# Kernel tuning notes

Measured on AMD Instinct MI355X. Metric: run time of the kernel, lower is better.

The kernel has to match this reference:

```python
import jax, jax.numpy as jnp
import numpy as np

N, E, H, L, G = 50000, 800000, 128, 4, 64

def setup_inputs() -> dict:
    key = jax.random.key(0)
    ks = jax.random.split(key, 16)
    s = 0.05
    x = jax.random.normal(ks[0], (N, H), jnp.float32)
    edge_index = jax.random.randint(ks[1], (2, E), 0, N)
    edge_attr = jax.random.normal(ks[2], (E, 1), jnp.float32)
    # sorted graph assignment covering all G graphs (batch[-1]+1 == G)
    batch = (jnp.arange(N) * G) // N
    conv_W1 = jax.random.normal(ks[3], (L, H, H), jnp.float32) * s
    conv_b1 = jnp.zeros((L, H), jnp.float32)
    conv_W2 = jax.random.normal(ks[4], (L, H, H), jnp.float32) * s
    conv_b2 = jnp.zeros((L, H), jnp.float32)
    conv_eps = jnp.zeros((L,), jnp.float32)  # torch init: eps = 0
    edge_W = jax.random.normal(ks[5], (L, 1, H), jnp.float32) * s
    edge_b = jnp.zeros((L, H), jnp.float32)
    vn_W1 = jax.random.normal(ks[6], (L - 1, H, H), jnp.float32) * s
    vn_b1 = jnp.zeros((L - 1, H), jnp.float32)
    vn_W2 = jax.random.normal(ks[7], (L - 1, H, H), jnp.float32) * s
    vn_b2 = jnp.zeros((L - 1, H), jnp.float32)
    vn_emb = jnp.zeros((H,), jnp.float32)  # torch init: constant 0
    return dict(x=x, edge_attr=edge_attr, conv_W1=conv_W1, conv_b1=conv_b1,
                conv_W2=conv_W2, conv_b2=conv_b2, conv_eps=conv_eps,
                edge_W=edge_W, edge_b=edge_b, vn_W1=vn_W1, vn_b1=vn_b1,
                vn_W2=vn_W2, vn_b2=vn_b2, vn_emb=vn_emb,
                edge_index=edge_index, batch=batch)


def reference(x, edge_attr, conv_W1, conv_b1, conv_W2, conv_b2, conv_eps,
              edge_W, edge_b, vn_W1, vn_b1, vn_W2, vn_b2, vn_emb,
              edge_index, batch):
    src, tgt = edge_index[0], edge_index[1]
    # PyG mean aggregation: divide scatter-sum by in-degree (clamped to 1)
    deg = jnp.maximum(
        jax.ops.segment_sum(jnp.ones((E,), x.dtype), tgt, num_segments=N), 1.0)[:, None]
    vn = jnp.broadcast_to(vn_emb[None, :], (G, H))  # virtual node per graph
    h = x
    hs = []
    for i in range(L):
        h = h + vn[batch]
        edge_emb = edge_attr @ edge_W[i] + edge_b[i]          # [E,H]
        msg = jax.nn.relu(h[src] + edge_emb)                   # gather + relu
        agg = jax.ops.segment_sum(msg, tgt, num_segments=N) / deg  # mean scatter
        z = (1.0 + conv_eps[i]) * h + agg
        h = jax.nn.relu(z @ conv_W1[i] + conv_b1[i]) @ conv_W2[i] + conv_b2[i]
        hs.append(h)
        if i < L - 1:
            vt = jax.ops.segment_sum(hs[i], batch, num_segments=G) + vn
            vn = jax.nn.relu(
                jax.nn.relu(vt @ vn_W1[i] + vn_b1[i]) @ vn_W2[i] + vn_b2[i])
            # eval mode: dropout is identity
    return jnp.concatenate(hs, axis=1)  # [N, L*H] jumping-knowledge concat
```

## Files before the change

### kernel.cpp

```cpp
#include <hip/hip_runtime.h>

#define NN 50000
#define EE 800000
#define HH 128
#define LL 4
#define GG 64
#define NR 50048

typedef short bf16x8 __attribute__((ext_vector_type(8)));
typedef float f32x4 __attribute__((ext_vector_type(4)));

__device__ __forceinline__ unsigned bf_round(float f) {
  unsigned u = __float_as_uint(f);
  return (u + 0x7fffu + ((u >> 16) & 1u)) >> 16;
}
__device__ __forceinline__ unsigned bf_pack2(float lo, float hi) {
  return bf_round(lo) | (bf_round(hi) << 16);
}

__global__ __launch_bounds__(256) void count_kernel(const int* __restrict__ tgt,
                                                    int* __restrict__ cnt, int E) {
  int e = blockIdx.x * 256 + threadIdx.x;
  if (e < E) atomicAdd(&cnt[tgt[e]], 1);
}

__global__ __launch_bounds__(256) void blocksum_kernel(const int* __restrict__ cnt,
                                                       int* __restrict__ bs, int N) {
  int i = blockIdx.x * 256 + threadIdx.x;
  int v = (i < N) ? cnt[i] : 0;
  __shared__ int sm[256];
  sm[threadIdx.x] = v;
  __syncthreads();
  for (int s = 128; s >= 1; s >>= 1) {
    if (threadIdx.x < s) sm[threadIdx.x] += sm[threadIdx.x + s];
    __syncthreads();
  }
  if (threadIdx.x == 0) bs[blockIdx.x] = sm[0];
}

__global__ __launch_bounds__(256) void bs_scan_kernel(int* __restrict__ bs, int nb) {
  __shared__ int sm[256];
  int t = threadIdx.x;
  int v = (t < nb) ? bs[t] : 0;
  sm[t] = v;
  __syncthreads();
  for (int off = 1; off < 256; off <<= 1) {
    int u = (t >= off) ? sm[t - off] : 0;
    __syncthreads();
    sm[t] += u;
    __syncthreads();
  }
  if (t < nb) bs[t] = sm[t] - v;
  if (t == 255) bs[nb] = sm[255];
}

__global__ __launch_bounds__(256) void blockscan_kernel(const int* __restrict__ cnt,
                                                        const int* __restrict__ bs,
                                                        int* __restrict__ rp, int N, int nb) {
  int b = blockIdx.x, t = threadIdx.x;
  int i = b * 256 + t;
  int v = (i < N) ? cnt[i] : 0;
  __shared__ int sm[256];
  sm[t] = v;
  __syncthreads();
  for (int off = 1; off < 256; off <<= 1) {
    int u = (t >= off) ? sm[t - off] : 0;
    __syncthreads();
    sm[t] += u;
    __syncthreads();
  }
  if (i < N) rp[i] = sm[t] - v + bs[b];
  if (b == 0 && t == 0) rp[N] = bs[nb];
}

__global__ __launch_bounds__(256) void scatter_kernel(const int* __restrict__ src,
                                                      const int* __restrict__ tgt,
                                                      const float* __restrict__ attr,
                                                      const int* __restrict__ rp,
                                                      int* __restrict__ cur,
                                                      int2* __restrict__ es, int E) {
  int e = blockIdx.x * 256 + threadIdx.x;
  if (e < E) {
    int t = tgt[e];
    int p = rp[t] + atomicAdd(&cur[t], 1);
    int2 rec;
    rec.x = src[e];
    rec.y = __float_as_int(attr[e]);
    es[p] = rec;
  }
}

__global__ __launch_bounds__(256) void vn_init_kernel(const float* __restrict__ emb,
                                                      float* __restrict__ vn, int total) {
  int i = blockIdx.x * 256 + threadIdx.x;
  if (i < total) vn[i] = emb[i & (HH - 1)];
}

__global__ __launch_bounds__(256) void wtconv_kernel(const float* __restrict__ W1,
                                                     const float* __restrict__ W2,
                                                     short* __restrict__ wt1,
                                                     short* __restrict__ wt2) {
  int idx = blockIdx.x * 256 + threadIdx.x;
  int m = idx >> 14;
  int r = idx & 16383;
  int n = r >> 7, k = r & 127;
  const float* W = (m < LL) ? (W1 + (size_t)m * 16384) : (W2 + (size_t)(m - LL) * 16384);
  short* D = (m < LL) ? (wt1 + (size_t)m * 16384) : (wt2 + (size_t)(m - LL) * 16384);
  D[n * 128 + k] = (short)bf_round(W[k * 128 + n]);
}

__global__ __launch_bounds__(256) void pack_kernel(const float4* __restrict__ hp, int pitch4,
                                                   const float4* __restrict__ vn,
                                                   const int* __restrict__ batch,
                                                   uint2* __restrict__ hbf, int N) {
  int idx = blockIdx.x * 256 + threadIdx.x;
  if (idx >= N * (HH / 4)) return;
  int n = idx >> 5;
  int c4 = idx & 31;
  int g = batch[n];
  float4 a = hp[(size_t)n * pitch4 + c4];
  float4 b = vn[g * 32 + c4];
  uint2 o;
  o.x = bf_pack2(a.x + b.x, a.y + b.y);
  o.y = bf_pack2(a.z + b.z, a.w + b.w);
  hbf[idx] = o;
}

__global__ __launch_bounds__(128) void agg_kernel(const unsigned* __restrict__ hbf,
                                                  const float2* __restrict__ hp2, int pitch2,
                                                  const float2* __restrict__ vn2,
                                                  const int* __restrict__ batch,
                                                  const int2* __restrict__ es,
                                                  const int* __restrict__ rp,
                                                  const float2* __restrict__ eW2,
                                                  const float2* __restrict__ eb2,
                                                  const float* __restrict__ epsp,
                                                  unsigned* __restrict__ zb, int N) {
  int wave = threadIdx.x >> 6;
  int lane = threadIdx.x & 63;
  int n = blockIdx.x * 2 + wave;
  if (n >= N) return;
  float2 ew = eW2[lane];
  float2 eb = eb2[lane];
  int rs = rp[n], re = rp[n + 1];
  float acc0 = 0.f, acc1 = 0.f;
  int k = rs;
  for (; k + 8 <= re; k += 8) {
    int2 e[8];
    unsigned p[8];
#pragma unroll
    for (int u = 0; u < 8; ++u) e[u] = es[k + u];
#pragma unroll
    for (int u = 0; u < 8; ++u) p[u] = hbf[((unsigned)e[u].x << 6) + lane];
#pragma unroll
    for (int u = 0; u < 8; ++u) {
      float a = __int_as_float(e[u].y);
      acc0 += fmaxf(__uint_as_float(p[u] << 16) + fmaf(a, ew.x, eb.x), 0.f);
      acc1 += fmaxf(__uint_as_float(p[u] & 0xffff0000u) + fmaf(a, ew.y, eb.y), 0.f);
    }
  }
  for (; k + 4 <= re; k += 4) {
    int2 e[4];
    unsigned p[4];
#pragma unroll
    for (int u = 0; u < 4; ++u) e[u] = es[k + u];
#pragma unroll
    for (int u = 0; u < 4; ++u) p[u] = hbf[((unsigned)e[u].x << 6) + lane];
#pragma unroll
    for (int u = 0; u < 4; ++u) {
      float a = __int_as_float(e[u].y);
      acc0 += fmaxf(__uint_as_float(p[u] << 16) + fmaf(a, ew.x, eb.x), 0.f);
      acc1 += fmaxf(__uint_as_float(p[u] & 0xffff0000u) + fmaf(a, ew.y, eb.y), 0.f);
    }
  }
  for (; k < re; ++k) {
    int2 e = es[k];
    unsigned p = hbf[((unsigned)e.x << 6) + lane];
    float a = __int_as_float(e.y);
    acc0 += fmaxf(__uint_as_float(p << 16) + fmaf(a, ew.x, eb.x), 0.f);
    acc1 += fmaxf(__uint_as_float(p & 0xffff0000u) + fmaf(a, ew.y, eb.y), 0.f);
  }
  int g = batch[n];
  float2 h = hp2[(size_t)n * pitch2 + lane];
  float2 v = vn2[(size_t)g * 64 + lane];
  float hs0 = h.x + v.x;
  float hs1 = h.y + v.y;
  float inv = 1.f / fmaxf((float)(re - rs), 1.f);
  float onep = 1.f + epsp[0];
  float o0 = fmaf(onep, hs0, acc0 * inv);
  float o1 = fmaf(onep, hs1, acc1 * inv);
  zb[(size_t)n * 64 + lane] = bf_pack2(o0, o1);
}

__global__ __launch_bounds__(256) void mlp_kernel(const unsigned* __restrict__ zb,
                                                  const short* __restrict__ wt1,
                                                  const float* __restrict__ b1,
                                                  const short* __restrict__ wt2,
                                                  const float* __restrict__ b2,
                                                  float* __restrict__ out, int layer, int N) {
  __shared__ char smem[64 * 272];
  int tid = threadIdx.x;
  int w = tid >> 6, lane = tid & 63;
  int l15 = lane & 15, q = lane >> 4;
  int row0 = blockIdx.x * 64;
  int wrow = w * 16;

  const uint4* z4 = (const uint4*)zb;
#pragma unroll
  for (int it = 0; it < 4; ++it) {
    int f = lane + it * 64;
    int r = f >> 4, c16 = f & 15;
    uint4 v = z4[(size_t)(row0 + wrow + r) * 16 + c16];
    *(uint4*)(&smem[(wrow + r) * 272 + c16 * 16]) = v;
  }

  f32x4 zero = {0.f, 0.f, 0.f, 0.f};
  f32x4 acc[8];
#pragma unroll
  for (int j = 0; j < 8; ++j) acc[j] = zero;

#pragma unroll
  for (int s = 0; s < 4; ++s) {
    bf16x8 af = *(const bf16x8*)(&smem[(wrow + l15) * 272 + (s * 32 + q * 8) * 2]);
#pragma unroll
    for (int j = 0; j < 8; ++j) {
      bf16x8 bf = *(const bf16x8*)(wt1 + (size_t)(j * 16 + l15) * 128 + s * 32 + q * 8);
      acc[j] = __builtin_amdgcn_mfma_f32_16x16x32_bf16(af, bf, acc[j], 0, 0, 0);
    }
  }
#pragma unroll
  for (int j = 0; j < 8; ++j) {
    float bv = b1[j * 16 + l15];
#pragma unroll
    for (int r = 0; r < 4; ++r) {
      float v = fmaxf(acc[j][r] + bv, 0.f);
      *(short*)(&smem[(wrow + q * 4 + r) * 272 + (j * 16 + l15) * 2]) = (short)bf_round(v);
    }
    acc[j] = zero;
  }
#pragma unroll
  for (int s = 0; s < 4; ++s) {
    bf16x8 af = *(const bf16x8*)(&smem[(wrow + l15) * 272 + (s * 32 + q * 8) * 2]);
#pragma unroll
    for (int j = 0; j < 8; ++j) {
      bf16x8 bf = *(const bf16x8*)(wt2 + (size_t)(j * 16 + l15) * 128 + s * 32 + q * 8);
      acc[j] = __builtin_amdgcn_mfma_f32_16x16x32_bf16(af, bf, acc[j], 0, 0, 0);
    }
  }
#pragma unroll
  for (int j = 0; j < 8; ++j) {
    float bv = b2[j * 16 + l15];
#pragma unroll
    for (int r = 0; r < 4; ++r) {
      int row = row0 + wrow + q * 4 + r;
      if (row < N)
        out[(size_t)row * (LL * HH) + layer * HH + j * 16 + l15] = acc[j][r] + bv;
    }
  }
}

__global__ __launch_bounds__(256) void gs_partial_kernel(const float* __restrict__ outbase,
                                                         float* __restrict__ part,
                                                         int N, int G) {
  int g = blockIdx.x >> 3, c = blockIdx.x & 7;
  int start = (int)(((long long)g * N + G - 1) / G);
  int end = (int)(((long long)(g + 1) * N + G - 1) / G);
  int len = end - start;
  int cs = start + (len * c) / 8;
  int ce = start + (len * (c + 1)) / 8;
  int c4 = threadIdx.x & 31;
  int rl = threadIdx.x >> 5;
  const float4* ob = (const float4*)outbase;
  float4 acc = make_float4(0.f, 0.f, 0.f, 0.f);
  for (int n = cs + rl; n < ce; n += 8) {
    float4 v = ob[(size_t)n * (LL * HH / 4) + c4];
    acc.x += v.x; acc.y += v.y; acc.z += v.z; acc.w += v.w;
  }
  __shared__ float4 sm[256];
  sm[threadIdx.x] = acc;
  __syncthreads();
  for (int s = 4; s >= 1; s >>= 1) {
    if (rl < s) {
      float4 o = sm[(rl + s) * 32 + c4];
      float4 m = sm[rl * 32 + c4];
      m.x += o.x; m.y += o.y; m.z += o.z; m.w += o.w;
      sm[rl * 32 + c4] = m;
    }
    __syncthreads();
  }
  if (rl == 0) ((float4*)part)[(size_t)blockIdx.x * 32 + c4] = sm[c4];
}

__global__ __launch_bounds__(128) void vn_fused_kernel(const float* __restrict__ part,
                                                       const float* __restrict__ W1,
                                                       const float* __restrict__ b1,
                                                       const float* __restrict__ W2,
                                                       const float* __restrict__ b2,
                                                       float* __restrict__ vn, int G) {
  int g = blockIdx.x, j = threadIdx.x;
  __shared__ float vr[128];
  __shared__ float tr[128];
  float s = vn[g * HH + j];
#pragma unroll
  for (int c = 0; c < 8; ++c) s += part[(size_t)(g * 8 + c) * HH + j];
  vr[j] = s;
  __syncthreads();
  float a = b1[j];
  for (int k = 0; k < 128; ++k) a = fmaf(vr[k], W1[k * HH + j], a);
  tr[j] = fmaxf(a, 0.f);
  __syncthreads();
  float o = b2[j];
  for (int k = 0; k < 128; ++k) o = fmaf(tr[k], W2[k * HH + j], o);
  vn[g * HH + j] = fmaxf(o, 0.f);
}

extern "C" void kernel_launch(void* const* d_in, const int* in_sizes, int n_in,
                              void* d_out, int out_size, void* d_ws, size_t ws_size,
                              hipStream_t stream) {
  const int N = NN, E = EE, H = HH, L = LL, G = GG;
  const float* x          = (const float*)d_in[0];
  const float* edge_attr  = (const float*)d_in[1];
  const float* conv_W1    = (const float*)d_in[2];
  const float* conv_b1    = (const float*)d_in[3];
  const float* conv_W2    = (const float*)d_in[4];
  const float* conv_b2    = (const float*)d_in[5];
  const float* conv_eps   = (const float*)d_in[6];
  const float* edge_W     = (const float*)d_in[7];
  const float* edge_b     = (const float*)d_in[8];
  const float* vn_W1      = (const float*)d_in[9];
  const float* vn_b1      = (const float*)d_in[10];
  const float* vn_W2      = (const float*)d_in[11];
  const float* vn_b2      = (const float*)d_in[12];
  const float* vn_emb     = (const float*)d_in[13];
  const int*   edge_index = (const int*)d_in[14];
  const int*   batch      = (const int*)d_in[15];
  float* out = (float*)d_out;

  const int nb = (N + 255) / 256;

  char* ws = (char*)d_ws;
  size_t off = 0;
  auto take = [&](size_t bytes) -> void* {
    void* p = ws + off;
    off = (off + bytes + 255) & ~(size_t)255;
    return p;
  };
  int*      cnt  = (int*)take((size_t)N * 4);
  int*      rp   = (int*)take((size_t)(N + 1) * 4);
  int*      bs   = (int*)take((size_t)(nb + 1) * 4);
  int2*     es   = (int2*)take((size_t)E * 8);
  unsigned* hbf  = (unsigned*)take((size_t)N * (H / 2) * 4);
  unsigned* zb   = (unsigned*)take((size_t)NR * (H / 2) * 4);
  short*    wt1  = (short*)take((size_t)L * H * H * 2);
  short*    wt2  = (short*)take((size_t)L * H * H * 2);
  float*    part = (float*)take((size_t)G * 8 * H * 4);
  float*    vn   = (float*)take((size_t)G * H * 4);

  const int* src = edge_index;
  const int* tgt = edge_index + E;

  hipMemsetAsync(cnt, 0, (size_t)N * 4, stream);
  count_kernel<<<(E + 255) / 256, 256, 0, stream>>>(tgt, cnt, E);
  blocksum_kernel<<<nb, 256, 0, stream>>>(cnt, bs, N);
  bs_scan_kernel<<<1, 256, 0, stream>>>(bs, nb);
  blockscan_kernel<<<nb, 256, 0, stream>>>(cnt, bs, rp, N, nb);
  hipMemsetAsync(cnt, 0, (size_t)N * 4, stream);
  scatter_kernel<<<(E + 255) / 256, 256, 0, stream>>>(src, tgt, edge_attr, rp, cnt, es, E);
  wtconv_kernel<<<(2 * L * H * H) / 256, 256, 0, stream>>>(conv_W1, conv_W2, wt1, wt2);
  vn_init_kernel<<<(G * H + 255) / 256, 256, 0, stream>>>(vn_emb, vn, G * H);

  for (int i = 0; i < L; ++i) {
    const float* hp;
    int pitch;
    if (i == 0) { hp = x; pitch = H; }
    else        { hp = out + (size_t)(i - 1) * H; pitch = L * H; }
    pack_kernel<<<(N * (H / 4) + 255) / 256, 256, 0, stream>>>(
        (const float4*)hp, pitch / 4, (const float4*)vn, batch, (uint2*)hbf, N);
    agg_kernel<<<(N + 1) / 2, 128, 0, stream>>>(
        hbf, (const float2*)hp, pitch / 2, (const float2*)vn, batch, es, rp,
        (const float2*)(edge_W + (size_t)i * H), (const float2*)(edge_b + (size_t)i * H),
        conv_eps + i, zb, N);
    mlp_kernel<<<NR / 64, 256, 0, stream>>>(
        zb, wt1 + (size_t)i * H * H, conv_b1 + (size_t)i * H,
        wt2 + (size_t)i * H * H, conv_b2 + (size_t)i * H, out, i, N);
    if (i < L - 1) {
      gs_partial_kernel<<<G * 8, 256, 0, stream>>>(out + (size_t)i * H, part, N, G);
      vn_fused_kernel<<<G, 128, 0, stream>>>(part, vn_W1 + (size_t)i * H * H,
                                             vn_b1 + (size_t)i * H,
                                             vn_W2 + (size_t)i * H * H,
                                             vn_b2 + (size_t)i * H, vn, G);
    }
  }
}
```

Baseline: 623.3 us.

## Vectorize edge gather, fuse graph-sum into MLP, merge init kernels

The aggregation kernel now splits each wave into four edge groups of 16 lanes, with each lane loading 8 bf16 features (uint4) per edge, and combines the groups with shuffles. Vector loads replace 4-byte ones and the scalar tail loops become a masked tail. The per-graph segment sum moves into the MLP epilogue as atomic adds into a single partial buffer, removing the separate gs_partial kernel and a re-read of the layer output. The memsets and small init kernels are folded into blockscan and one init kernel to cut launches, at the cost of float atomic contention and nondeterministic summation order.

Measured after the change: 621.1 us. Within noise of the previous version (-0.3%).

```diff
diff --git a/kernel.cpp b/kernel.cpp
--- a/kernel.cpp
+++ b/kernel.cpp
@@ -56,7 +56,8 @@
 
 __global__ __launch_bounds__(256) void blockscan_kernel(const int* __restrict__ cnt,
                                                         const int* __restrict__ bs,
-                                                        int* __restrict__ rp, int N, int nb) {
+                                                        int* __restrict__ rp,
+                                                        int* __restrict__ cur, int N, int nb) {
   int b = blockIdx.x, t = threadIdx.x;
   int i = b * 256 + t;
   int v = (i < N) ? cnt[i] : 0;
@@ -69,7 +70,7 @@
     sm[t] += u;
     __syncthreads();
   }
-  if (i < N) rp[i] = sm[t] - v + bs[b];
+  if (i < N) { rp[i] = sm[t] - v + bs[b]; cur[i] = 0; }
   if (b == 0 && t == 0) rp[N] = bs[nb];
 }
 
@@ -90,23 +91,28 @@
   }
 }
 
-__global__ __launch_bounds__(256) void vn_init_kernel(const float* __restrict__ emb,
-                                                      float* __restrict__ vn, int total) {
-  int i = blockIdx.x * 256 + threadIdx.x;
-  if (i < total) vn[i] = emb[i & (HH - 1)];
-}
-
-__global__ __launch_bounds__(256) void wtconv_kernel(const float* __restrict__ W1,
-                                                     const float* __restrict__ W2,
-                                                     short* __restrict__ wt1,
-                                                     short* __restrict__ wt2) {
+__global__ __launch_bounds__(256) void init_kernel(const float* __restrict__ W1,
+                                                   const float* __restrict__ W2,
+                                                   const float* __restrict__ emb,
+                                                   short* __restrict__ wt1,
+                                                   short* __restrict__ wt2,
+                                                   float* __restrict__ vn,
+                                                   float* __restrict__ part) {
   int idx = blockIdx.x * 256 + threadIdx.x;
-  int m = idx >> 14;
-  int r = idx & 16383;
-  int n = r >> 7, k = r & 127;
-  const float* W = (m < LL) ? (W1 + (size_t)m * 16384) : (W2 + (size_t)(m - LL) * 16384);
-  short* D = (m < LL) ? (wt1 + (size_t)m * 16384) : (wt2 + (size_t)(m - LL) * 16384);
-  D[n * 128 + k] = (short)bf_round(W[k * 128 + n]);
+  const int NW = 2 * LL * HH * HH;
+  if (idx < NW) {
+    int m = idx >> 14;
+    int r = idx & 16383;
+    int n = r >> 7, k = r & 127;
+    const float* W = (m < LL) ? (W1 + (size_t)m * 16384) : (W2 + (size_t)(m - LL) * 16384);
+    short* D = (m < LL) ? (wt1 + (size_t)m * 16384) : (wt2 + (size_t)(m - LL) * 16384);
+    D[n * 128 + k] = (short)bf_round(W[k * 128 + n]);
+  } else if (idx < NW + GG * HH) {
+    int i = idx - NW;
+    vn[i] = emb[i & (HH - 1)];
+  } else if (idx < NW + 2 * GG * HH) {
+    part[idx - NW - GG * HH] = 0.f;
+  }
 }
 
 __global__ __launch_bounds__(256) void pack_kernel(const float4* __restrict__ hp, int pitch4,
@@ -126,70 +132,88 @@
   hbf[idx] = o;
 }
 
-__global__ __launch_bounds__(128) void agg_kernel(const unsigned* __restrict__ hbf,
-                                                  const float2* __restrict__ hp2, int pitch2,
-                                                  const float2* __restrict__ vn2,
+__device__ __forceinline__ void accum8(float* acc, uint4 p, float a,
+                                       const float4& ew0, const float4& ew1,
+                                       const float4& eb0, const float4& eb1, float m) {
+  float lo, hi;
+  lo = __uint_as_float(p.x << 16); hi = __uint_as_float(p.x & 0xffff0000u);
+  acc[0] += m * fmaxf(lo + fmaf(a, ew0.x, eb0.x), 0.f);
+  acc[1] += m * fmaxf(hi + fmaf(a, ew0.y, eb0.y), 0.f);
+  lo = __uint_as_float(p.y << 16); hi = __uint_as_float(p.y & 0xffff0000u);
+  acc[2] += m * fmaxf(lo + fmaf(a, ew0.z, eb0.z), 0.f);
+  acc[3] += m * fmaxf(hi + fmaf(a, ew0.w, eb0.w), 0.f);
+  lo = __uint_as_float(p.z << 16); hi = __uint_as_float(p.z & 0xffff0000u);
+  acc[4] += m * fmaxf(lo + fmaf(a, ew1.x, eb1.x), 0.f);
+  acc[5] += m * fmaxf(hi + fmaf(a, ew1.y, eb1.y), 0.f);
+  lo = __uint_as_float(p.w << 16); hi = __uint_as_float(p.w & 0xffff0000u);
+  acc[6] += m * fmaxf(lo + fmaf(a, ew1.z, eb1.z), 0.f);
+  acc[7] += m * fmaxf(hi + fmaf(a, ew1.w, eb1.w), 0.f);
+}
+
+__global__ __launch_bounds__(128) void agg_kernel(const uint4* __restrict__ hbf4,
+                                                  const float* __restrict__ hp, int pitch,
+                                                  const float* __restrict__ vnp,
                                                   const int* __restrict__ batch,
                                                   const int2* __restrict__ es,
                                                   const int* __restrict__ rp,
-                                                  const float2* __restrict__ eW2,
-                                                  const float2* __restrict__ eb2,
+                                                  const float* __restrict__ eW,
+                                                  const float* __restrict__ eb,
                                                   const float* __restrict__ epsp,
-                                                  unsigned* __restrict__ zb, int N) {
+                                                  uint4* __restrict__ zb4, int N) {
   int wave = threadIdx.x >> 6;
   int lane = threadIdx.x & 63;
   int n = blockIdx.x * 2 + wave;
   if (n >= N) return;
-  float2 ew = eW2[lane];
-  float2 eb = eb2[lane];
+  int q = lane >> 4;
+  int c = lane & 15;
+  float4 ew0 = *(const float4*)(eW + c * 8);
+  float4 ew1 = *(const float4*)(eW + c * 8 + 4);
+  float4 eb0 = *(const float4*)(eb + c * 8);
+  float4 eb1 = *(const float4*)(eb + c * 8 + 4);
   int rs = rp[n], re = rp[n + 1];
-  float acc0 = 0.f, acc1 = 0.f;
+  float acc[8];
+#pragma unroll
+  for (int j = 0; j < 8; ++j) acc[j] = 0.f;
   int k = rs;
   for (; k + 8 <= re; k += 8) {
-    int2 e[8];
-    unsigned p[8];
-#pragma unroll
-    for (int u = 0; u < 8; ++u) e[u] = es[k + u];
-#pragma unroll
-    for (int u = 0; u < 8; ++u) p[u] = hbf[((unsigned)e[u].x << 6) + lane];
-#pragma unroll
-    for (int u = 0; u < 8; ++u) {
-      float a = __int_as_float(e[u].y);
-      acc0 += fmaxf(__uint_as_float(p[u] << 16) + fmaf(a, ew.x, eb.x), 0.f);
-      acc1 += fmaxf(__uint_as_float(p[u] & 0xffff0000u) + fmaf(a, ew.y, eb.y), 0.f);
-    }
-  }
-  for (; k + 4 <= re; k += 4) {
-    int2 e[4];
-    unsigned p[4];
-#pragma unroll
-    for (int u = 0; u < 4; ++u) e[u] = es[k + u];
-#pragma unroll
-    for (int u = 0; u < 4; ++u) p[u] = hbf[((unsigned)e[u].x << 6) + lane];
-#pragma unroll
-    for (int u = 0; u < 4; ++u) {
-      float a = __int_as_float(e[u].y);
-      acc0 += fmaxf(__uint_as_float(p[u] << 16) + fmaf(a, ew.x, eb.x), 0.f);
-      acc1 += fmaxf(__uint_as_float(p[u] & 0xffff0000u) + fmaf(a, ew.y, eb.y), 0.f);
-    }
-  }
-  for (; k < re; ++k) {
-    int2 e = es[k];
-    unsigned p = hbf[((unsigned)e.x << 6) + lane];
-    float a = __int_as_float(e.y);
-    acc0 += fmaxf(__uint_as_float(p << 16) + fmaf(a, ew.x, eb.x), 0.f);
-    acc1 += fmaxf(__uint_as_float(p & 0xffff0000u) + fmaf(a, ew.y, eb.y), 0.f);
+    int2 e0 = es[k + q];
+    int2 e1 = es[k + 4 + q];
+    uint4 p0 = hbf4[(size_t)e0.x * 16 + c];
+    uint4 p1 = hbf4[(size_t)e1.x * 16 + c];
+    accum8(acc, p0, __int_as_float(e0.y), ew0, ew1, eb0, eb1, 1.f);
+    accum8(acc, p1, __int_as_float(e1.y), ew0, ew1, eb0, eb1, 1.f);
+  }
+  for (; k < re; k += 4) {
+    int idx = min(k + q, re - 1);
+    int2 e = es[idx];
+    float m = (k + q < re) ? 1.f : 0.f;
+    uint4 p = hbf4[(size_t)e.x * 16 + c];
+    accum8(acc, p, __int_as_float(e.y), ew0, ew1, eb0, eb1, m);
+  }
+#pragma unroll
+  for (int j = 0; j < 8; ++j) {
+    acc[j] += __shfl_xor(acc[j], 16);
+    acc[j] += __shfl_xor(acc[j], 32);
   }
   int g = batch[n];
-  float2 h = hp2[(size_t)n * pitch2 + lane];
-  float2 v = vn2[(size_t)g * 64 + lane];
-  float hs0 = h.x + v.x;
-  float hs1 = h.y + v.y;
+  const float* hrow = hp + (size_t)n * pitch + c * 8;
+  const float* vrow = vnp + g * HH + c * 8;
+  float4 h0 = *(const float4*)(hrow);
+  float4 h1 = *(const float4*)(hrow + 4);
+  float4 v0 = *(const float4*)(vrow);
+  float4 v1 = *(const float4*)(vrow + 4);
   float inv = 1.f / fmaxf((float)(re - rs), 1.f);
   float onep = 1.f + epsp[0];
-  float o0 = fmaf(onep, hs0, acc0 * inv);
-  float o1 = fmaf(onep, hs1, acc1 * inv);
-  zb[(size_t)n * 64 + lane] = bf_pack2(o0, o1);
+  uint4 o;
+  o.x = bf_pack2(fmaf(onep, h0.x + v0.x, acc[0] * inv),
+                 fmaf(onep, h0.y + v0.y, acc[1] * inv));
+  o.y = bf_pack2(fmaf(onep, h0.z + v0.z, acc[2] * inv),
+                 fmaf(onep, h0.w + v0.w, acc[3] * inv));
+  o.z = bf_pack2(fmaf(onep, h1.x + v1.x, acc[4] * inv),
+                 fmaf(onep, h1.y + v1.y, acc[5] * inv));
+  o.w = bf_pack2(fmaf(onep, h1.z + v1.z, acc[6] * inv),
+                 fmaf(onep, h1.w + v1.w, acc[7] * inv));
+  if (q == 0) zb4[(size_t)n * 16 + c] = o;
 }
 
 __global__ __launch_bounds__(256) void mlp_kernel(const unsigned* __restrict__ zb,
@@ -197,7 +221,9 @@
                                                   const float* __restrict__ b1,
                                                   const short* __restrict__ wt2,
                                                   const float* __restrict__ b2,
-                                                  float* __restrict__ out, int layer, int N) {
+                                                  float* __restrict__ out,
+                                                  float* __restrict__ part,
+                                                  int do_gs, int layer, int N) {
   __shared__ char smem[64 * 272];
   int tid = threadIdx.x;
   int w = tid >> 6, lane = tid & 63;
@@ -247,51 +273,35 @@
       acc[j] = __builtin_amdgcn_mfma_f32_16x16x32_bf16(af, bf, acc[j], 0, 0, 0);
     }
   }
+  int g0 = (int)(((long long)row0 * GG) / NN);
 #pragma unroll
   for (int j = 0; j < 8; ++j) {
     float bv = b2[j * 16 + l15];
+    float s0 = 0.f, s1 = 0.f;
 #pragma unroll
     for (int r = 0; r < 4; ++r) {
       int row = row0 + wrow + q * 4 + r;
-      if (row < N)
-        out[(size_t)row * (LL * HH) + layer * HH + j * 16 + l15] = acc[j][r] + bv;
-    }
-  }
-}
-
-__global__ __launch_bounds__(256) void gs_partial_kernel(const float* __restrict__ outbase,
-                                                         float* __restrict__ part,
-                                                         int N, int G) {
-  int g = blockIdx.x >> 3, c = blockIdx.x & 7;
-  int start = (int)(((long long)g * N + G - 1) / G);
-  int end = (int)(((long long)(g + 1) * N + G - 1) / G);
-  int len = end - start;
-  int cs = start + (len * c) / 8;
-  int ce = start + (len * (c + 1)) / 8;
-  int c4 = threadIdx.x & 31;
-  int rl = threadIdx.x >> 5;
-  const float4* ob = (const float4*)outbase;
-  float4 acc = make_float4(0.f, 0.f, 0.f, 0.f);
-  for (int n = cs + rl; n < ce; n += 8) {
-    float4 v = ob[(size_t)n * (LL * HH / 4) + c4];
-    acc.x += v.x; acc.y += v.y; acc.z += v.z; acc.w += v.w;
-  }
-  __shared__ float4 sm[256];
-  sm[threadIdx.x] = acc;
-  __syncthreads();
-  for (int s = 4; s >= 1; s >>= 1) {
-    if (rl < s) {
-      float4 o = sm[(rl + s) * 32 + c4];
-      float4 m = sm[rl * 32 + c4];
-      m.x += o.x; m.y += o.y; m.z += o.z; m.w += o.w;
-      sm[rl * 32 + c4] = m;
-    }
-    __syncthreads();
-  }
-  if (rl == 0) ((float4*)part)[(size_t)blockIdx.x * 32 + c4] = sm[c4];
-}
-
-__global__ __launch_bounds__(128) void vn_fused_kernel(const float* __restrict__ part,
+      if (row < N) {
+        float v = acc[j][r] + bv;
+        out[(size_t)row * (LL * HH) + layer * HH + j * 16 + l15] = v;
+        if (do_gs) {
+          int rel = (int)(((long long)row * GG) / NN) - g0;
+          if (rel == 0) s0 += v; else s1 += v;
+        }
+      }
+    }
+    if (do_gs) {
+      s0 += __shfl_xor(s0, 16); s0 += __shfl_xor(s0, 32);
+      s1 += __shfl_xor(s1, 16); s1 += __shfl_xor(s1, 32);
+      if (q == 0) {
+        atomicAdd(&part[g0 * HH + j * 16 + l15], s0);
+        if (s1 != 0.f) atomicAdd(&part[(g0 + 1) * HH + j * 16 + l15], s1);
+      }
+    }
+  }
+}
+
+__global__ __launch_bounds__(128) void vn_fused_kernel(float* __restrict__ part,
                                                        const float* __restrict__ W1,
                                                        const float* __restrict__ b1,
                                                        const float* __restrict__ W2,
@@ -300,10 +310,8 @@
   int g = blockIdx.x, j = threadIdx.x;
   __shared__ float vr[128];
   __shared__ float tr[128];
-  float s = vn[g * HH + j];
-#pragma unroll
-  for (int c = 0; c < 8; ++c) s += part[(size_t)(g * 8 + c) * HH + j];
-  vr[j] = s;
+  vr[j] = vn[g * HH + j] + part[g * HH + j];
+  part[g * HH + j] = 0.f;
   __syncthreads();
   float a = b1[j];
   for (int k = 0; k < 128; ++k) a = fmaf(vr[k], W1[k * HH + j], a);
@@ -346,6 +354,7 @@
     return p;
   };
   int*      cnt  = (int*)take((size_t)N * 4);
+  int*      cur  = (int*)take((size_t)N * 4);
   int*      rp   = (int*)take((size_t)(N + 1) * 4);
   int*      bs   = (int*)take((size_t)(nb + 1) * 4);
   int2*     es   = (int2*)take((size_t)E * 8);
@@ -353,7 +362,7 @@
   unsigned* zb   = (unsigned*)take((size_t)NR * (H / 2) * 4);
   short*    wt1  = (short*)take((size_t)L * H * H * 2);
   short*    wt2  = (short*)take((size_t)L * H * H * 2);
-  float*    part = (float*)take((size_t)G * 8 * H * 4);
+  float*    part = (float*)take((size_t)G * H * 4);
   float*    vn   = (float*)take((size_t)G * H * 4);
 
   const int* src = edge_index;
@@ -363,11 +372,10 @@
   count_kernel<<<(E + 255) / 256, 256, 0, stream>>>(tgt, cnt, E);
   blocksum_kernel<<<nb, 256, 0, stream>>>(cnt, bs, N);
   bs_scan_kernel<<<1, 256, 0, stream>>>(bs, nb);
-  blockscan_kernel<<<nb, 256, 0, stream>>>(cnt, bs, rp, N, nb);
-  hipMemsetAsync(cnt, 0, (size_t)N * 4, stream);
-  scatter_kernel<<<(E + 255) / 256, 256, 0, stream>>>(src, tgt, edge_attr, rp, cnt, es, E);
-  wtconv_kernel<<<(2 * L * H * H) / 256, 256, 0, stream>>>(conv_W1, conv_W2, wt1, wt2);
-  vn_init_kernel<<<(G * H + 255) / 256, 256, 0, stream>>>(vn_emb, vn, G * H);
+  blockscan_kernel<<<nb, 256, 0, stream>>>(cnt, bs, rp, cur, N, nb);
+  scatter_kernel<<<(E + 255) / 256, 256, 0, stream>>>(src, tgt, edge_attr, rp, cur, es, E);
+  init_kernel<<<(2 * L * H * H + 2 * G * H + 255) / 256, 256, 0, stream>>>(
+      conv_W1, conv_W2, vn_emb, wt1, wt2, vn, part);
 
   for (int i = 0; i < L; ++i) {
     const float* hp;
@@ -377,14 +385,14 @@
     pack_kernel<<<(N * (H / 4) + 255) / 256, 256, 0, stream>>>(
         (const float4*)hp, pitch / 4, (const float4*)vn, batch, (uint2*)hbf, N);
     agg_kernel<<<(N + 1) / 2, 128, 0, stream>>>(
-        hbf, (const float2*)hp, pitch / 2, (const float2*)vn, batch, es, rp,
-        (const float2*)(edge_W + (size_t)i * H), (const float2*)(edge_b + (size_t)i * H),
-        conv_eps + i, zb, N);
+        (const uint4*)hbf, hp, pitch, vn, batch, es, rp,
+        edge_W + (size_t)i * H, edge_b + (size_t)i * H,
+        conv_eps + i, (uint4*)zb, N);
     mlp_kernel<<<NR / 64, 256, 0, stream>>>(
         zb, wt1 + (size_t)i * H * H, conv_b1 + (size_t)i * H,
-        wt2 + (size_t)i * H * H, conv_b2 + (size_t)i * H, out, i, N);
+        wt2 + (size_t)i * H * H, conv_b2 + (size_t)i * H, out, part,
+        (i < L - 1) ? 1 : 0, i, N);
     if (i < L - 1) {
-      gs_partial_kernel<<<G * 8, 256, 0, stream>>>(out + (size_t)i * H, part, N, G);
       vn_fused_kernel<<<G, 128, 0, stream>>>(part, vn_W1 + (size_t)i * H * H,
                                              vn_b1 + (size_t)i * H,
                                              vn_W2 + (size_t)i * H * H,
```
